# Performance work log

Measured on AMD Instinct MI355X. Metric: run time of the kernel, lower is better.

## Reference

```python
import jax, jax.numpy as jnp
import numpy as np

S, T, B = 1024, 64, 8
KEY_DIM, QUERY_DIM, HIDDEN = 512, 512, 256


def setup_inputs() -> dict:
    key = jax.random.key(0)
    ks = jax.random.split(key, 8)
    inp = {
        "key": jax.random.normal(ks[0], (S, B, KEY_DIM), dtype=jnp.float32),
        "query": jax.random.normal(ks[1], (T, B, QUERY_DIM), dtype=jnp.float32),
        # torch nn.Linear params, stored as (in, out) for x @ W
        "Wk": jax.random.normal(ks[2], (KEY_DIM, HIDDEN), dtype=jnp.float32) * (1.0 / np.sqrt(KEY_DIM)),
        "bk": jax.random.normal(ks[3], (HIDDEN,), dtype=jnp.float32) * 0.01,
        "Wq": jax.random.normal(ks[4], (QUERY_DIM, HIDDEN), dtype=jnp.float32) * (1.0 / np.sqrt(QUERY_DIM)),
        "bq": jax.random.normal(ks[5], (HIDDEN,), dtype=jnp.float32) * 0.01,
        "v": jax.random.normal(ks[6], (HIDDEN,), dtype=jnp.float32),
    }
    return inp


def reference(key, query, Wk, bk, Wq, bq, v):
    # key: (S, B, Dk), query: (T, B, Dq)
    key_proj = key @ Wk + bk          # (S, B, H)
    query_proj = query @ Wq + bq      # (T, B, H)
    # broadcast add: (T,1,B,H) + (1,S,B,H) -> (T,S,B,H)
    energy = jnp.tanh(query_proj[:, None, :, :] + key_proj[None, :, :, :])
    scores = jnp.einsum('tsbh,h->tsb', energy, v)  # (T, S, B)
    attn = jax.nn.softmax(scores, axis=1)          # softmax over key positions S
    return jnp.transpose(attn, (2, 0, 1))          # (B, T, S)
```

## Files before the change

### kernel.cpp

```cpp
#include <hip/hip_runtime.h>

#define S_DIM 1024
#define T_DIM 64
#define B_DIM 8
#define K_DIM 512
#define H_DIM 256

typedef _Float16 f16;
typedef __attribute__((ext_vector_type(4))) _Float16 f16x4;
typedef __attribute__((ext_vector_type(8))) _Float16 f16x8;
typedef __attribute__((ext_vector_type(4))) float f32x4;

__device__ __forceinline__ float fast_rcp(float x) { return __builtin_amdgcn_rcpf(x); }

__device__ __forceinline__ void gload16(const void* g, void* l) {
    __builtin_amdgcn_global_load_lds(
        (const __attribute__((address_space(1))) unsigned int*)g,
        (__attribute__((address_space(3))) unsigned int*)l, 16, 0, 0);
}

__global__ __launch_bounds__(256) void wconv_kernel(
    const float* __restrict__ Wk, const float* __restrict__ Wq,
    f16* __restrict__ WTk, f16* __restrict__ WTq)
{
    __shared__ float tile[64][65];
    const int idx = blockIdx.x;
    const float* W = (idx & 32) ? Wq : Wk;
    f16* WT = (idx & 32) ? WTq : WTk;
    const int t32 = idx & 31;
    const int k0 = (t32 >> 2) * 64, n0 = (t32 & 3) * 64;
    const int c = threadIdx.x & 63, r0 = threadIdx.x >> 6;
#pragma unroll
    for (int i = 0; i < 16; ++i) {
        int r = r0 + i * 4;
        tile[r][c] = W[(size_t)(k0 + r) * H_DIM + n0 + c];
    }
    __syncthreads();
#pragma unroll
    for (int i = 0; i < 16; ++i) {
        int r = r0 + i * 4;
        WT[(size_t)(n0 + r) * K_DIM + k0 + c] = (f16)tile[c][r];
    }
}

__global__ __launch_bounds__(256, 4) void proj_gemm_all(
    const float* __restrict__ key, const f16* __restrict__ WTk,
    const float* __restrict__ bk, float* __restrict__ ktT,
    const float* __restrict__ query, const f16* __restrict__ WTq,
    const float* __restrict__ bq, float* __restrict__ tq2)
{
    __shared__ __align__(16) char smem[2][16384];
    const int tid = threadIdx.x;
    const int lane = tid & 63, wid = tid >> 6;
    const int widu = __builtin_amdgcn_readfirstlane(wid);
    const int wm = (wid >> 1) * 16, wn = (wid & 1) * 32;

    const int bid0 = blockIdx.x;
    const int bid = (bid0 & 7) * 136 + (bid0 >> 3);
    const bool isQ = bid >= 1024;
    const int lb = isQ ? bid - 1024 : bid;
    const size_t m0 = (size_t)(lb >> 2) * 32;
    const int n0 = (lb & 3) * 64;
    const float* A    = isQ ? query : key;
    const f16* BT     = isQ ? WTq : WTk;
    const float* bias = isQ ? bq : bk;
    float* P          = isQ ? tq2 : ktT;

    const int o0 = tid << 4;
    const int o1 = o0 + 4096;
    const int row0 = o0 >> 7, kb0 = (o0 & 127) ^ ((row0 & 7) << 4);
    const int row1 = o1 >> 7, kb1 = (o1 & 127) ^ ((row1 & 7) << 4);
    const char* b_t = (const char*)(BT + (size_t)n0 * K_DIM);

    auto GLOADB = [&](int buf, int t) {
        const int kb = t * 128;
        char* d0 = &smem[buf][8192 + widu * 1024];
        gload16(b_t + (size_t)row0 * 1024 + kb + kb0, d0);
        gload16(b_t + (size_t)row1 * 1024 + kb + kb1, d0 + 4096);
    };

    const float* a_base = A + m0 * K_DIM;
    float4 areg[2];
    auto ALOAD = [&](int t) {
#pragma unroll
        for (int j = 0; j < 2; ++j) {
            const int fidx = j * 256 + tid;
            const int r = fidx >> 4, c16 = fidx & 15;
            areg[j] = *(const float4*)&a_base[(size_t)r * K_DIM + t * 64 + c16 * 4];
        }
    };
    auto AWRITE = [&](int buf) {
#pragma unroll
        for (int j = 0; j < 2; ++j) {
            const int fidx = j * 256 + tid;
            const int r = fidx >> 4, c16 = fidx & 15;
            const int byt = r * 128 + ((c16 * 8) ^ ((r & 7) << 4));
            f16 h0 = (f16)areg[j].x, h1 = (f16)areg[j].y, h2 = (f16)areg[j].z, h3 = (f16)areg[j].w;
            f16x4 hi = {h0, h1, h2, h3};
            f16x4 lo = {(f16)(areg[j].x - (float)h0), (f16)(areg[j].y - (float)h1),
                        (f16)(areg[j].z - (float)h2), (f16)(areg[j].w - (float)h3)};
            *(f16x4*)&smem[buf][byt] = hi;
            *(f16x4*)&smem[buf][4096 + byt] = lo;
        }
    };

    f32x4 acc[2] = {};
    const int fr = lane & 15, fgb = (lane >> 4) << 4;

    auto COMPUTE = [&](int buf) {
#pragma unroll
        for (int kk = 0; kk < 2; ++kk) {
            const int kbyte = kk * 64 + fgb;
            const int arow = wm + fr;
            const int abyt = (arow << 7) + (kbyte ^ ((arow & 7) << 4));
            f16x8 ah = *(const f16x8*)&smem[buf][abyt];
            f16x8 al = *(const f16x8*)&smem[buf][4096 + abyt];
            const int brow0 = wn + fr, brow1 = wn + 16 + fr;
            f16x8 b0 = *(const f16x8*)&smem[buf][8192 + (brow0 << 7) + (kbyte ^ ((brow0 & 7) << 4))];
            f16x8 b1 = *(const f16x8*)&smem[buf][8192 + (brow1 << 7) + (kbyte ^ ((brow1 & 7) << 4))];
            acc[0] = __builtin_amdgcn_mfma_f32_16x16x32_f16(ah, b0, acc[0], 0, 0, 0);
            acc[1] = __builtin_amdgcn_mfma_f32_16x16x32_f16(ah, b1, acc[1], 0, 0, 0);
            acc[0] = __builtin_amdgcn_mfma_f32_16x16x32_f16(al, b0, acc[0], 0, 0, 0);
            acc[1] = __builtin_amdgcn_mfma_f32_16x16x32_f16(al, b1, acc[1], 0, 0, 0);
        }
    };

    ALOAD(0);
    GLOADB(0, 0);
    AWRITE(0);
    __syncthreads();

    int buf = 0;
#pragma unroll 1
    for (int t = 0; t < 8; ++t) {
        if (t < 7) { ALOAD(t + 1); GLOADB(buf ^ 1, t + 1); }
        COMPUTE(buf);
        if (t < 7) { AWRITE(buf ^ 1); __syncthreads(); }
        buf ^= 1;
    }

    const int crow = (lane >> 4) * 4, ccol = lane & 15;
#pragma unroll
    for (int g = 0; g < 2; ++g) {
        int col = n0 + wn + g * 16 + ccol;
        float bv = bias[col];
#pragma unroll
        for (int r = 0; r < 4; ++r) {
            size_t row = m0 + wm + crow + r;
            float val = __expf(2.0f * (acc[g][r] + bv));
            if (!isQ)
                P[((size_t)(row & 7) * H_DIM + col) * S_DIM + (row >> 3)] = val;
            else
                P[((size_t)(row & 7) * T_DIM + (row >> 3)) * H_DIM + col] = val;
        }
    }
}

__global__ __launch_bounds__(256) void scores_kernel(
    const float* __restrict__ ktT, const float* __restrict__ tq2,
    const float* __restrict__ v, float* __restrict__ scores)
{
    const int tid = threadIdx.x, lane = tid & 63;
    const int wid = __builtin_amdgcn_readfirstlane(tid >> 6);
    const int bb = blockIdx.x;
    const int b = bb & 7;
    const int sblk = (bb >> 3) & 15;
    const int t0 = ((bb >> 7) << 3) + wid * 2;
    const int s = sblk * 64 + lane;

    const float* kcol = ktT + (size_t)b * H_DIM * S_DIM + s;
    const float* q0p = tq2 + ((size_t)b * T_DIM + t0) * H_DIM;
    const float* q1p = q0p + H_DIM;

    float a0 = 0.f, a1 = 0.f;
#pragma unroll 8
    for (int h = 0; h < H_DIM; ++h) {
        float k  = kcol[(size_t)h * S_DIM];
        float q0 = q0p[h], q1 = q1p[h];
        float vv = v[h];
        a0 = fmaf(vv, fast_rcp(fmaf(q0, k, 1.0f)), a0);
        a1 = fmaf(vv, fast_rcp(fmaf(q1, k, 1.0f)), a1);
    }
    float* so = scores + ((size_t)b * T_DIM + t0) * S_DIM + s;
    so[0]     = -2.0f * a0;
    so[S_DIM] = -2.0f * a1;
}

__global__ __launch_bounds__(256) void softmax_kernel(
    const float* __restrict__ scores, float* __restrict__ out)
{
    const int row = blockIdx.x;
    const int lane = threadIdx.x & 63;
    const int wave = threadIdx.x >> 6;
    __shared__ float red[8];

    float4 x = ((const float4*)(scores + (size_t)row * S_DIM))[threadIdx.x];
    float m = fmaxf(fmaxf(x.x, x.y), fmaxf(x.z, x.w));
#pragma unroll
    for (int mm = 32; mm >= 1; mm >>= 1) m = fmaxf(m, __shfl_xor(m, mm, 64));
    if (lane == 0) red[wave] = m;
    __syncthreads();
    m = fmaxf(fmaxf(red[0], red[1]), fmaxf(red[2], red[3]));

    float e0 = __expf(x.x - m), e1 = __expf(x.y - m);
    float e2 = __expf(x.z - m), e3 = __expf(x.w - m);
    float sum = e0 + e1 + e2 + e3;
#pragma unroll
    for (int mm = 32; mm >= 1; mm >>= 1) sum += __shfl_xor(sum, mm, 64);
    if (lane == 0) red[4 + wave] = sum;
    __syncthreads();
    float inv = fast_rcp(red[4] + red[5] + red[6] + red[7]);

    float4 o;
    o.x = e0 * inv; o.y = e1 * inv; o.z = e2 * inv; o.w = e3 * inv;
    ((float4*)(out + (size_t)row * S_DIM))[threadIdx.x] = o;
}

extern "C" void kernel_launch(void* const* d_in, const int* in_sizes, int n_in,
                              void* d_out, int out_size, void* d_ws, size_t ws_size,
                              hipStream_t stream)
{
    const float* key   = (const float*)d_in[0];
    const float* query = (const float*)d_in[1];
    const float* Wk    = (const float*)d_in[2];
    const float* bk    = (const float*)d_in[3];
    const float* Wq    = (const float*)d_in[4];
    const float* bq    = (const float*)d_in[5];
    const float* v     = (const float*)d_in[6];
    float* out = (float*)d_out;

    float* ktT    = (float*)d_ws;
    float* tq2    = ktT + (size_t)B_DIM * H_DIM * S_DIM;
    float* scores = tq2 + (size_t)B_DIM * T_DIM * H_DIM;
    f16* WTk = (f16*)(scores + (size_t)B_DIM * T_DIM * S_DIM);
    f16* WTq = WTk + (size_t)H_DIM * K_DIM;

    wconv_kernel<<<64, 256, 0, stream>>>(Wk, Wq, WTk, WTq);
    proj_gemm_all<<<1088, 256, 0, stream>>>(key, WTk, bk, ktT, query, WTq, bq, tq2);
    scores_kernel<<<1024, 256, 0, stream>>>(ktT, tq2, v, scores);
    softmax_kernel<<<B_DIM * T_DIM, 256, 0, stream>>>(scores, out);
}
```

Measured before the change: 52.52 us.

## Double projection GEMM M-tile and stage key-projection output through LDS for coalesced stores

The projection GEMM tile grows from 32x64 to 64x64, so each wave computes a 2x2 grid of MFMA fragments. This halves the block count and improves reuse of the B operand loaded into LDS. The key-projection epilogue now writes the tile to shared memory and then emits coalesced float4 stores in the transposed ktT layout, replacing scattered scalar stores. The cost is more LDS and registers per block, with the occupancy hint lowered to 3, and an extra barrier in the epilogue.

```diff
diff --git a/kernel.cpp b/kernel.cpp
--- a/kernel.cpp
+++ b/kernel.cpp
@@ -43,30 +43,29 @@
     }
 }
 
-__global__ __launch_bounds__(256, 4) void proj_gemm_all(
+__global__ __launch_bounds__(256, 3) void proj_gemm_all(
     const float* __restrict__ key, const f16* __restrict__ WTk,
     const float* __restrict__ bk, float* __restrict__ ktT,
     const float* __restrict__ query, const f16* __restrict__ WTq,
     const float* __restrict__ bq, float* __restrict__ tq2)
 {
-    __shared__ __align__(16) char smem[2][16384];
+    __shared__ __align__(16) char smem[2][3][8192];
     const int tid = threadIdx.x;
     const int lane = tid & 63, wid = tid >> 6;
     const int widu = __builtin_amdgcn_readfirstlane(wid);
-    const int wm = (wid >> 1) * 16, wn = (wid & 1) * 32;
+    const int wm = (wid >> 1) * 32, wn = (wid & 1) * 32;
 
     const int bid0 = blockIdx.x;
-    const int bid = (bid0 & 7) * 136 + (bid0 >> 3);
-    const bool isQ = bid >= 1024;
-    const int lb = isQ ? bid - 1024 : bid;
-    const size_t m0 = (size_t)(lb >> 2) * 32;
+    const int bid = (bid0 & 7) * 68 + (bid0 >> 3);
+    const bool isQ = bid >= 512;
+    const int lb = isQ ? bid - 512 : bid;
+    const size_t m0 = (size_t)(lb >> 2) * 64;
     const int n0 = (lb & 3) * 64;
     const float* A    = isQ ? query : key;
     const f16* BT     = isQ ? WTq : WTk;
     const float* bias = isQ ? bq : bk;
-    float* P          = isQ ? tq2 : ktT;
-
-    const int o0 = tid << 4;
+
+    const int o0 = wid * 1024 + (lane << 4);
     const int o1 = o0 + 4096;
     const int row0 = o0 >> 7, kb0 = (o0 & 127) ^ ((row0 & 7) << 4);
     const int row1 = o1 >> 7, kb1 = (o1 & 127) ^ ((row1 & 7) << 4);
@@ -74,16 +73,16 @@
 
     auto GLOADB = [&](int buf, int t) {
         const int kb = t * 128;
-        char* d0 = &smem[buf][8192 + widu * 1024];
+        char* d0 = &smem[buf][2][widu * 1024];
         gload16(b_t + (size_t)row0 * 1024 + kb + kb0, d0);
         gload16(b_t + (size_t)row1 * 1024 + kb + kb1, d0 + 4096);
     };
 
     const float* a_base = A + m0 * K_DIM;
-    float4 areg[2];
+    float4 areg[4];
     auto ALOAD = [&](int t) {
 #pragma unroll
-        for (int j = 0; j < 2; ++j) {
+        for (int j = 0; j < 4; ++j) {
             const int fidx = j * 256 + tid;
             const int r = fidx >> 4, c16 = fidx & 15;
             areg[j] = *(const float4*)&a_base[(size_t)r * K_DIM + t * 64 + c16 * 4];
@@ -91,7 +90,7 @@
     };
     auto AWRITE = [&](int buf) {
 #pragma unroll
-        for (int j = 0; j < 2; ++j) {
+        for (int j = 0; j < 4; ++j) {
             const int fidx = j * 256 + tid;
             const int r = fidx >> 4, c16 = fidx & 15;
             const int byt = r * 128 + ((c16 * 8) ^ ((r & 7) << 4));
@@ -99,29 +98,33 @@
             f16x4 hi = {h0, h1, h2, h3};
             f16x4 lo = {(f16)(areg[j].x - (float)h0), (f16)(areg[j].y - (float)h1),
                         (f16)(areg[j].z - (float)h2), (f16)(areg[j].w - (float)h3)};
-            *(f16x4*)&smem[buf][byt] = hi;
-            *(f16x4*)&smem[buf][4096 + byt] = lo;
-        }
-    };
-
-    f32x4 acc[2] = {};
+            *(f16x4*)&smem[buf][0][byt] = hi;
+            *(f16x4*)&smem[buf][1][byt] = lo;
+        }
+    };
+
+    f32x4 acc[2][2] = {};
     const int fr = lane & 15, fgb = (lane >> 4) << 4;
 
     auto COMPUTE = [&](int buf) {
 #pragma unroll
         for (int kk = 0; kk < 2; ++kk) {
             const int kbyte = kk * 64 + fgb;
-            const int arow = wm + fr;
-            const int abyt = (arow << 7) + (kbyte ^ ((arow & 7) << 4));
-            f16x8 ah = *(const f16x8*)&smem[buf][abyt];
-            f16x8 al = *(const f16x8*)&smem[buf][4096 + abyt];
-            const int brow0 = wn + fr, brow1 = wn + 16 + fr;
-            f16x8 b0 = *(const f16x8*)&smem[buf][8192 + (brow0 << 7) + (kbyte ^ ((brow0 & 7) << 4))];
-            f16x8 b1 = *(const f16x8*)&smem[buf][8192 + (brow1 << 7) + (kbyte ^ ((brow1 & 7) << 4))];
-            acc[0] = __builtin_amdgcn_mfma_f32_16x16x32_f16(ah, b0, acc[0], 0, 0, 0);
-            acc[1] = __builtin_amdgcn_mfma_f32_16x16x32_f16(ah, b1, acc[1], 0, 0, 0);
-            acc[0] = __builtin_amdgcn_mfma_f32_16x16x32_f16(al, b0, acc[0], 0, 0, 0);
-            acc[1] = __builtin_amdgcn_mfma_f32_16x16x32_f16(al, b1, acc[1], 0, 0, 0);
+            auto ld = [&](int arr, int row) -> f16x8 {
+                int byt = ((row << 7) + kbyte) ^ ((row & 7) << 4);
+                return *(const f16x8*)&smem[buf][arr][byt];
+            };
+            f16x8 ah0 = ld(0, wm + fr),      ah1 = ld(0, wm + 16 + fr);
+            f16x8 al0 = ld(1, wm + fr),      al1 = ld(1, wm + 16 + fr);
+            f16x8 b0  = ld(2, wn + fr),      b1  = ld(2, wn + 16 + fr);
+            acc[0][0] = __builtin_amdgcn_mfma_f32_16x16x32_f16(ah0, b0, acc[0][0], 0, 0, 0);
+            acc[0][1] = __builtin_amdgcn_mfma_f32_16x16x32_f16(ah0, b1, acc[0][1], 0, 0, 0);
+            acc[1][0] = __builtin_amdgcn_mfma_f32_16x16x32_f16(ah1, b0, acc[1][0], 0, 0, 0);
+            acc[1][1] = __builtin_amdgcn_mfma_f32_16x16x32_f16(ah1, b1, acc[1][1], 0, 0, 0);
+            acc[0][0] = __builtin_amdgcn_mfma_f32_16x16x32_f16(al0, b0, acc[0][0], 0, 0, 0);
+            acc[0][1] = __builtin_amdgcn_mfma_f32_16x16x32_f16(al0, b1, acc[0][1], 0, 0, 0);
+            acc[1][0] = __builtin_amdgcn_mfma_f32_16x16x32_f16(al1, b0, acc[1][0], 0, 0, 0);
+            acc[1][1] = __builtin_amdgcn_mfma_f32_16x16x32_f16(al1, b1, acc[1][1], 0, 0, 0);
         }
     };
 
@@ -140,18 +143,46 @@
     }
 
     const int crow = (lane >> 4) * 4, ccol = lane & 15;
-#pragma unroll
-    for (int g = 0; g < 2; ++g) {
-        int col = n0 + wn + g * 16 + ccol;
-        float bv = bias[col];
-#pragma unroll
-        for (int r = 0; r < 4; ++r) {
-            size_t row = m0 + wm + crow + r;
-            float val = __expf(2.0f * (acc[g][r] + bv));
-            if (!isQ)
-                P[((size_t)(row & 7) * H_DIM + col) * S_DIM + (row >> 3)] = val;
-            else
-                P[((size_t)(row & 7) * T_DIM + (row >> 3)) * H_DIM + col] = val;
+    if (isQ) {
+#pragma unroll
+        for (int f = 0; f < 2; ++f)
+#pragma unroll
+            for (int g = 0; g < 2; ++g) {
+                int col = n0 + wn + g * 16 + ccol;
+                float bv = bias[col];
+#pragma unroll
+                for (int r = 0; r < 4; ++r) {
+                    size_t row = m0 + wm + f * 16 + crow + r;
+                    float val = __expf(2.0f * (acc[f][g][r] + bv));
+                    tq2[((size_t)(row & 7) * T_DIM + (row >> 3)) * H_DIM + col] = val;
+                }
+            }
+    } else {
+        float* lt = (float*)&smem[0][0][0];
+#pragma unroll
+        for (int f = 0; f < 2; ++f)
+#pragma unroll
+            for (int g = 0; g < 2; ++g) {
+                int lcol = wn + g * 16 + ccol;
+                float bv = bias[n0 + lcol];
+#pragma unroll
+                for (int r = 0; r < 4; ++r) {
+                    int lrow = wm + f * 16 + crow + r;
+                    lt[lrow * 64 + lcol] = __expf(2.0f * (acc[f][g][r] + bv));
+                }
+            }
+        __syncthreads();
+        const int sbase = (int)(m0 >> 3);
+#pragma unroll
+        for (int p = 0; p < 4; ++p) {
+            int c = p * 256 + tid;
+            int h = c & 63, b2 = (c >> 6) & 7, sq = c >> 9;
+            float4 o;
+            o.x = lt[((sq * 4 + 0) * 8 + b2) * 64 + h];
+            o.y = lt[((sq * 4 + 1) * 8 + b2) * 64 + h];
+            o.z = lt[((sq * 4 + 2) * 8 + b2) * 64 + h];
+            o.w = lt[((sq * 4 + 3) * 8 + b2) * 64 + h];
+            *(float4*)&ktT[((size_t)b2 * H_DIM + n0 + h) * S_DIM + sbase + sq * 4] = o;
         }
     }
 }
@@ -236,7 +267,7 @@
     f16* WTq = WTk + (size_t)H_DIM * K_DIM;
 
     wconv_kernel<<<64, 256, 0, stream>>>(Wk, Wq, WTk, WTq);
-    proj_gemm_all<<<1088, 256, 0, stream>>>(key, WTk, bk, ktT, query, WTq, bq, tq2);
+    proj_gemm_all<<<544, 256, 0, stream>>>(key, WTk, bk, ktT, query, WTq, bq, tq2);
     scores_kernel<<<1024, 256, 0, stream>>>(ktT, tq2, v, scores);
     softmax_kernel<<<B_DIM * T_DIM, 256, 0, stream>>>(scores, out);
 }
```

Measured after the change: 49.46 us. 1.06x faster.

## Stage key projection transpose through LDS and pair reciprocals in scores loop

Applied to the files above, without the earlier changes.

The key-projection epilogue now writes the tile to shared memory first, then emits float4 stores along S into the transposed ktT layout, replacing strided scalar scatter stores. The scores kernel combines two h terms as va/A + vb/B = (va*B + vb*A)/(A*B), halving the reciprocal count at the cost of extra multiplies. The pairing risks overflow or precision loss when the products of exp-domain values get large.

```diff
diff --git a/kernel.cpp b/kernel.cpp
--- a/kernel.cpp
+++ b/kernel.cpp
@@ -64,7 +64,6 @@
     const float* A    = isQ ? query : key;
     const f16* BT     = isQ ? WTq : WTk;
     const float* bias = isQ ? bq : bk;
-    float* P          = isQ ? tq2 : ktT;
 
     const int o0 = tid << 4;
     const int o1 = o0 + 4096;
@@ -133,25 +132,55 @@
     int buf = 0;
 #pragma unroll 1
     for (int t = 0; t < 8; ++t) {
-        if (t < 7) { ALOAD(t + 1); GLOADB(buf ^ 1, t + 1); }
+        if (t < 7) {
+            ALOAD(t + 1);
+            GLOADB(buf ^ 1, t + 1);
+        }
         COMPUTE(buf);
-        if (t < 7) { AWRITE(buf ^ 1); __syncthreads(); }
+        if (t < 7) {
+            AWRITE(buf ^ 1);
+            __syncthreads();
+        }
         buf ^= 1;
     }
 
     const int crow = (lane >> 4) * 4, ccol = lane & 15;
-#pragma unroll
-    for (int g = 0; g < 2; ++g) {
-        int col = n0 + wn + g * 16 + ccol;
-        float bv = bias[col];
-#pragma unroll
-        for (int r = 0; r < 4; ++r) {
-            size_t row = m0 + wm + crow + r;
-            float val = __expf(2.0f * (acc[g][r] + bv));
-            if (!isQ)
-                P[((size_t)(row & 7) * H_DIM + col) * S_DIM + (row >> 3)] = val;
-            else
-                P[((size_t)(row & 7) * T_DIM + (row >> 3)) * H_DIM + col] = val;
+    if (isQ) {
+#pragma unroll
+        for (int g = 0; g < 2; ++g) {
+            int col = n0 + wn + g * 16 + ccol;
+            float bv = bias[col];
+#pragma unroll
+            for (int r = 0; r < 4; ++r) {
+                size_t row = m0 + wm + crow + r;
+                float val = __expf(2.0f * (acc[g][r] + bv));
+                tq2[((size_t)(row & 7) * T_DIM + (row >> 3)) * H_DIM + col] = val;
+            }
+        }
+    } else {
+        float* lt = (float*)&smem[0][0];
+#pragma unroll
+        for (int g = 0; g < 2; ++g) {
+            int lcol = wn + g * 16 + ccol;
+            float bv = bias[n0 + lcol];
+#pragma unroll
+            for (int r = 0; r < 4; ++r) {
+                int lrow = wm + crow + r;
+                lt[lrow * 64 + lcol] = __expf(2.0f * (acc[g][r] + bv));
+            }
+        }
+        __syncthreads();
+        const int sbase = (int)(m0 >> 3);
+#pragma unroll
+        for (int p = 0; p < 2; ++p) {
+            int c = p * 256 + tid;
+            int h = c & 63, b2 = c >> 6;
+            float4 o;
+            o.x = lt[(0 * 8 + b2) * 64 + h];
+            o.y = lt[(1 * 8 + b2) * 64 + h];
+            o.z = lt[(2 * 8 + b2) * 64 + h];
+            o.w = lt[(3 * 8 + b2) * 64 + h];
+            *(float4*)&ktT[((size_t)b2 * H_DIM + n0 + h) * S_DIM + sbase] = o;
         }
     }
 }
@@ -171,17 +200,23 @@
     const float* kcol = ktT + (size_t)b * H_DIM * S_DIM + s;
     const float* q0p = tq2 + ((size_t)b * T_DIM + t0) * H_DIM;
     const float* q1p = q0p + H_DIM;
+    float* so = scores + ((size_t)b * T_DIM + t0) * S_DIM + s;
 
     float a0 = 0.f, a1 = 0.f;
 #pragma unroll 8
-    for (int h = 0; h < H_DIM; ++h) {
-        float k  = kcol[(size_t)h * S_DIM];
-        float q0 = q0p[h], q1 = q1p[h];
-        float vv = v[h];
-        a0 = fmaf(vv, fast_rcp(fmaf(q0, k, 1.0f)), a0);
-        a1 = fmaf(vv, fast_rcp(fmaf(q1, k, 1.0f)), a1);
-    }
-    float* so = scores + ((size_t)b * T_DIM + t0) * S_DIM + s;
+    for (int h = 0; h < H_DIM; h += 2) {
+        float k0 = kcol[(size_t)h * S_DIM];
+        float k1 = kcol[(size_t)(h + 1) * S_DIM];
+        float va = v[h], vb = v[h + 1];
+        float q0a = q0p[h], q0b = q0p[h + 1];
+        float q1a = q1p[h], q1b = q1p[h + 1];
+        float A0 = fmaf(q0a, k0, 1.0f), B0 = fmaf(q0b, k1, 1.0f);
+        float A1 = fmaf(q1a, k0, 1.0f), B1 = fmaf(q1b, k1, 1.0f);
+        float n0 = fmaf(va, B0, vb * A0);
+        float n1 = fmaf(va, B1, vb * A1);
+        a0 = fmaf(n0, fast_rcp(A0 * B0), a0);
+        a1 = fmaf(n1, fast_rcp(A1 * B1), a1);
+    }
     so[0]     = -2.0f * a0;
     so[S_DIM] = -2.0f * a1;
 }
```

Measured after the change: 47.56 us. 9.4% less time.
